# Kernel tuning notes

Hardware: AMD Instinct MI355X
Metric: run time of the kernel (lower is better)

Reference implementation:

```python
import jax, jax.numpy as jnp
import numpy as np
from jax import lax

B, T1, E, D, OUT = 4096, 127, 128, 128, 1


def setup_inputs() -> dict:
    key = jax.random.key(0)
    ks = jax.random.split(key, 16)
    s = lambda fan_in: 1.0 / np.sqrt(fan_in)
    inp = {
        "input_encoded": jax.random.normal(ks[0], (B, T1, E), jnp.float32),
        "y_history": jax.random.normal(ks[1], (B, T1), jnp.float32),
        # v_d: Linear(E -> 1)
        "v_d_w": jax.random.uniform(ks[2], (1, E), jnp.float32, -s(E), s(E)),
        "v_d_b": jax.random.uniform(ks[3], (1,), jnp.float32, -s(E), s(E)),
        # W_dhs: Linear(2D -> E)
        "W_dhs_w": jax.random.uniform(ks[4], (E, 2 * D), jnp.float32, -s(2 * D), s(2 * D)),
        "W_dhs_b": jax.random.uniform(ks[5], (E,), jnp.float32, -s(2 * D), s(2 * D)),
        # U_d: Linear(E -> E)
        "U_d_w": jax.random.uniform(ks[6], (E, E), jnp.float32, -s(E), s(E)),
        "U_d_b": jax.random.uniform(ks[7], (E,), jnp.float32, -s(E), s(E)),
        # w: Linear((1+E)*OUT -> OUT); torch code does w.weight.data.normal_()
        "w_w": jax.random.normal(ks[8], (OUT, (1 + E) * OUT), jnp.float32),
        "w_b": jax.random.uniform(ks[9], (OUT,), jnp.float32, -s((1 + E) * OUT), s((1 + E) * OUT)),
        # single-layer LSTM(input=OUT, hidden=D); gate order i,f,g,o
        "lstm_W_ih": jax.random.uniform(ks[10], (4 * D, OUT), jnp.float32, -s(D), s(D)),
        "lstm_W_hh": jax.random.uniform(ks[11], (4 * D, D), jnp.float32, -s(D), s(D)),
        "lstm_b_ih": jax.random.uniform(ks[12], (4 * D,), jnp.float32, -s(D), s(D)),
        "lstm_b_hh": jax.random.uniform(ks[13], (4 * D,), jnp.float32, -s(D), s(D)),
        # fc_final: Linear(D + OUT*E -> OUT)
        "fc_w": jax.random.uniform(ks[14], (OUT, D + OUT * E), jnp.float32, -s(D + OUT * E), s(D + OUT * E)),
        "fc_b": jax.random.uniform(ks[15], (OUT,), jnp.float32, -s(D + OUT * E), s(D + OUT * E)),
    }
    return inp


def reference(input_encoded, y_history, v_d_w, v_d_b, W_dhs_w, W_dhs_b,
              U_d_w, U_d_b, w_w, w_b, lstm_W_ih, lstm_W_hh, lstm_b_ih,
              lstm_b_hh, fc_w, fc_b):
    batch = input_encoded.shape[0]
    d = lstm_W_hh.shape[1]
    e = input_encoded.shape[2]
    # U_d applied to encoder outputs is step-independent: precompute once. [B,T1,E]
    U = input_encoded @ U_d_w.T + U_d_b

    def step(carry, y_t):
        h, c, _ = carry  # h,c: [B,D]
        # temporal attention over encoder timesteps
        proj = jnp.concatenate([h, c], axis=-1) @ W_dhs_w.T + W_dhs_b  # [B,E]
        scores = jnp.tanh(proj[:, None, :] + U) @ v_d_w[0] + v_d_b[0]  # [B,T1]
        beta = jax.nn.softmax(scores, axis=1)
        ctx = jnp.einsum('bt,bte->be', beta, input_encoded)  # [B,E]
        # y_tilde and one LSTM step
        y_tilde = jnp.concatenate([ctx, y_t[:, None]], axis=-1) @ w_w.T + w_b  # [B,1]
        gates = y_tilde @ lstm_W_ih.T + lstm_b_ih + h @ lstm_W_hh.T + lstm_b_hh
        i_g, f_g, g_g, o_g = jnp.split(gates, 4, axis=-1)
        c_new = jax.nn.sigmoid(f_g) * c + jax.nn.sigmoid(i_g) * jnp.tanh(g_g)
        h_new = jax.nn.sigmoid(o_g) * jnp.tanh(c_new)
        return (h_new, c_new, ctx), None

    h0 = jnp.zeros((batch, d), input_encoded.dtype)
    c0 = jnp.zeros((batch, d), input_encoded.dtype)
    ctx0 = jnp.zeros((batch, e), input_encoded.dtype)
    (h, c, ctx), _ = lax.scan(step, (h0, c0, ctx0), y_history.T)  # scan over T-1 steps
    y_pred = jnp.concatenate([h, ctx], axis=-1) @ fc_w.T + fc_b  # [B,1]
    return y_pred
```

## Files before the change

### kernel.cpp

```cpp
#include <hip/hip_runtime.h>
#include <hip/hip_bf16.h>

#if __has_builtin(__builtin_amdgcn_exp2f)
#define EXP2F(x) __builtin_amdgcn_exp2f(x)
#else
#define EXP2F(x) exp2f(x)
#endif
#if __has_builtin(__builtin_amdgcn_rcpf)
#define RCPF(x) __builtin_amdgcn_rcpf(x)
#else
#define RCPF(x) (1.0f/(x))
#endif

typedef _Float16 h2f16 __attribute__((ext_vector_type(2)));
typedef _Float16 f16x8 __attribute__((ext_vector_type(8)));
typedef float    f32x16 __attribute__((ext_vector_type(16)));

namespace {
constexpr int   kT   = 127;
constexpr int   kE   = 128;
constexpr int   kB   = 4096;
constexpr int   kNWG = 256;
constexpr int   kGRP = 4;
constexpr int   kBPW = 16;
constexpr float kLog2e = 1.4426950408889634f;
constexpr float kK2    = 2.8853900817779268f;
constexpr int   kSmemBytes = (32768 + 256 + 672) * 4 + (2064 + 6 * 512 + 128 + 256 + 132) * 4;

__device__ __forceinline__ unsigned int packf16(float a, float b) {
  h2f16 h = { (_Float16)a, (_Float16)b };
  return __builtin_bit_cast(unsigned int, h);
}

#if __has_builtin(__builtin_amdgcn_fdot2)
__device__ __forceinline__ float fdot2f(unsigned int a, unsigned int b, float c) {
  return __builtin_amdgcn_fdot2(__builtin_bit_cast(h2f16, a),
                                __builtin_bit_cast(h2f16, b), c, false);
}
#else
__device__ __forceinline__ float fdot2f(unsigned int a, unsigned int b, float c) {
  h2f16 ha = __builtin_bit_cast(h2f16, a), hb = __builtin_bit_cast(h2f16, b);
  return c + (float)ha.x * (float)hb.x + (float)ha.y * (float)hb.y;
}
#endif

template <int CTRL>
__device__ __forceinline__ float dppadd(float x) {
  return x + __int_as_float(__builtin_amdgcn_update_dpp(
      0, __float_as_int(x), CTRL, 0xF, 0xF, true));
}
template <int CTRL>
__device__ __forceinline__ float dppmov(float x) {
  return __int_as_float(__builtin_amdgcn_update_dpp(
      0, __float_as_int(x), CTRL, 0xF, 0xF, true));
}
__device__ __forceinline__ float redsum8dpp(float x) {
  x = dppadd<0xB1>(x); x = dppadd<0x4E>(x); x = dppadd<0x141>(x);
  return x;
}
__device__ __forceinline__ float redsum64dpp(float x) {
  x = dppadd<0xB1>(x); x = dppadd<0x4E>(x); x = dppadd<0x141>(x); x = dppadd<0x128>(x);
  x += __shfl_xor(x, 16, 64);
  x += __shfl_xor(x, 32, 64);
  return x;
}
__device__ __forceinline__ float redsum64(float a) {
#pragma unroll
  for (int m = 1; m < 64; m <<= 1) a += __shfl_xor(a, m, 64);
  return a;
}

__global__ __launch_bounds__(1024, 4) void decoder_kernel(
    const float* __restrict__ Xg,
    const float* __restrict__ yh,
    const float* __restrict__ vdw,
    const float* __restrict__ vdb,
    const float* __restrict__ Wdhs,
    const float* __restrict__ Wdhsb,
    const float* __restrict__ Udw,
    const float* __restrict__ Udb,
    const float* __restrict__ ww,
    const float* __restrict__ wb,
    const float* __restrict__ Wih,
    const float* __restrict__ Whh,
    const float* __restrict__ bih,
    const float* __restrict__ bhh,
    const float* __restrict__ fcww,
    const float* __restrict__ fcb,
    float* __restrict__ out)
{
  extern __shared__ char smem[];
  unsigned int* u2u  = (unsigned int*)smem;
  unsigned int* udw2 = u2u + 3 * 8192;
  unsigned int* p2h  = u2u + 4 * 8192;
  unsigned int* hc2  = p2h + 256;
  float* act  = (float*)(hc2 + 672);
  float* sc   = act  + 2064;
  float* XW   = sc   + 512;
  float* yc   = XW   + 512;
  float* beta = yc   + 512;
  float* hl   = beta + 512;
  float* ctxl = hl   + 512;
  float* udbl = ctxl + 512;
  float* fcw  = udbl + 128;
  float* wwl  = fcw  + 256;

  const int tid   = threadIdx.x;
  const int d8    = tid >> 3;
  const int sub   = tid & 7;
  const int gate  = sub >> 1;
  const int g     = gate * 128 + d8;
  const int lane  = tid & 63;

  unsigned int whhA[32];
  {
    const int wid = tid >> 6;
    const int rrA = lane & 31;
    const int rowA = (rrA & 3) * 128 + (8 * wid + (rrA >> 2));
    const int kbA = (lane >> 5) * 8;
#pragma unroll
    for (int kk = 0; kk < 8; ++kk)
#pragma unroll
      for (int i2 = 0; i2 < 4; ++i2) {
        const int k = kk * 16 + kbA + 2 * i2;
        whhA[kk * 4 + i2] = packf16(Whh[rowA * 128 + k], Whh[rowA * 128 + k + 1]);
      }
  }
  unsigned int wdq[16];
#pragma unroll
  for (int q = 0; q < 16; ++q)
    wdq[q] = packf16(Wdhs[d8 * 256 + sub * 32 + 2 * q],
                     Wdhs[d8 * 256 + sub * 32 + 2 * q + 1]);
  unsigned int v2p[8];
#pragma unroll
  for (int i = 0; i < 8; ++i)
    v2p[i] = packf16(-2.0f * vdw[sub * 16 + 2 * i], -2.0f * vdw[sub * 16 + 2 * i + 1]);
  float bihh = bih[g] + bhh[g];
  float wihr = Wih[g];
  float wdbp = Wdhsb[d8];
  const float a_c = (gate == 2) ? -2.0f : 1.0f;
  const float b_c = (gate == 2) ? kK2 : -kLog2e;
  const float c_c = (gate == 2) ? 1.0f : 0.0f;
#pragma unroll
  for (int p = 0; p < 32; ++p) asm volatile("" : "+v"(whhA[p]));
#pragma unroll
  for (int q = 0; q < 16; ++q) asm volatile("" : "+v"(wdq[q]));
#pragma unroll
  for (int i = 0; i < 8; ++i) asm volatile("" : "+v"(v2p[i]));
  asm volatile("" : "+v"(bihh));
  asm volatile("" : "+v"(wihr));
  asm volatile("" : "+v"(wdbp));

  if (tid < 132) wwl[tid] = (tid < 129) ? ww[tid] : ((tid == 129) ? wb[0] : 0.f);
  if (tid < 256) fcw[tid] = fcww[tid];
  if (tid < 128) udbl[tid] = Udb[tid];
  (void)vdb;

  for (int grp = 0; grp < kBPW / kGRP; ++grp) {
    const int b0 = blockIdx.x * kBPW + grp * kGRP;
    float creg[kGRP] = {0.f, 0.f, 0.f, 0.f};
    __syncthreads();

    {
      const int r = tid >> 3, mb = (tid & 7) * 2;
#pragma unroll
      for (int ch = 0; ch < 2; ++ch) {
        const int m = mb + ch;
        const float4 wa = *(const float4*)&Udw[r * kE + m * 8];
        const float4 wb4 = *(const float4*)&Udw[r * kE + m * 8 + 4];
        uint4 st;
        st.x = packf16(wa.x, wa.y);  st.y = packf16(wa.z, wa.w);
        st.z = packf16(wb4.x, wb4.y); st.w = packf16(wb4.z, wb4.w);
        *(uint4*)&udw2[r * 64 + ((m ^ (r >> 4)) << 2)] = st;
      }
    }
    if (tid < 672) hc2[tid] = 0u;
    if (tid < 512) {
      const int j = tid >> 7, s2 = tid & 127;
      yc[tid] = (s2 < kT) ? wwl[128] * yh[(size_t)(b0 + j) * kT + s2] + wwl[129] : 0.f;
      if (s2 == 127) XW[tid] = 0.f;
    }
    __syncthreads();

    uint4 st3a, st3b;
    if (d8 < kT) {
#pragma unroll
      for (int j = 0; j < kGRP; ++j) {
        const float* Xrow = Xg + (size_t)(b0 + j) * (kT * kE) + d8 * kE;
        float a = 0.f;
#pragma unroll
        for (int q = 0; q < 4; ++q) {
          const float4 xv = *(const float4*)&Xrow[sub * 16 + q * 4];
          const float4 wv = *(const float4*)&wwl[sub * 16 + q * 4];
          a += xv.x * wv.x + xv.y * wv.y + xv.z * wv.z + xv.w * wv.w;
        }
        a = redsum8dpp(a);
        if (sub == 0) XW[j * 128 + d8] = a;
        float acc[16];
#pragma unroll
        for (int jj = 0; jj < 16; ++jj) acc[jj] = 0.f;
        for (int m = 0; m < 16; ++m) {
          const float4 xa = *(const float4*)&Xrow[m * 8];
          const float4 xb4 = *(const float4*)&Xrow[m * 8 + 4];
          const unsigned int xp0 = packf16(xa.x, xa.y), xp1 = packf16(xa.z, xa.w);
          const unsigned int xp2 = packf16(xb4.x, xb4.y), xp3 = packf16(xb4.z, xb4.w);
#pragma unroll
          for (int jj = 0; jj < 16; ++jj) {
            const uint4 wq = *(const uint4*)&udw2[(sub * 16 + jj) * 64 + ((m ^ sub) << 2)];
            acc[jj] = fdot2f(xp3, wq.w, fdot2f(xp2, wq.z,
                      fdot2f(xp1, wq.y, fdot2f(xp0, wq.x, acc[jj]))));
          }
        }
        uint4 s0, s1;
        const int eb = sub * 16;
        s0.x = packf16(kK2 * (acc[0] + udbl[eb + 0]), kK2 * (acc[1] + udbl[eb + 1]));
        s0.y = packf16(kK2 * (acc[2] + udbl[eb + 2]), kK2 * (acc[3] + udbl[eb + 3]));
        s0.z = packf16(kK2 * (acc[4] + udbl[eb + 4]), kK2 * (acc[5] + udbl[eb + 5]));
        s0.w = packf16(kK2 * (acc[6] + udbl[eb + 6]), kK2 * (acc[7] + udbl[eb + 7]));
        s1.x = packf16(kK2 * (acc[8] + udbl[eb + 8]), kK2 * (acc[9] + udbl[eb + 9]));
        s1.y = packf16(kK2 * (acc[10] + udbl[eb + 10]), kK2 * (acc[11] + udbl[eb + 11]));
        s1.z = packf16(kK2 * (acc[12] + udbl[eb + 12]), kK2 * (acc[13] + udbl[eb + 13]));
        s1.w = packf16(kK2 * (acc[14] + udbl[eb + 14]), kK2 * (acc[15] + udbl[eb + 15]));
        if (j < 3) {
          *(uint4*)&u2u[j * 8192 + d8 * 64 + (((sub * 2 + 0) ^ (d8 & 15)) << 2)] = s0;
          *(uint4*)&u2u[j * 8192 + d8 * 64 + (((sub * 2 + 1) ^ (d8 & 15)) << 2)] = s1;
        } else { st3a = s0; st3b = s1; }
      }
    }
    __syncthreads();
    if (d8 < kT) {
      *(uint4*)&u2u[3 * 8192 + d8 * 64 + (((sub * 2 + 0) ^ (d8 & 15)) << 2)] = st3a;
      *(uint4*)&u2u[3 * 8192 + d8 * 64 + (((sub * 2 + 1) ^ (d8 & 15)) << 2)] = st3b;
    }

    for (int s = 0; s < kT; ++s) {
      {
        f32x16 macc;
#pragma unroll
        for (int i = 0; i < 16; ++i) macc[i] = 0.f;
        const int jn = tid & 3;
        const int hi4 = ((tid >> 5) & 1) * 4;
#pragma unroll
        for (int kk = 0; kk < 8; ++kk) {
          const int p0 = kk * 8 + hi4;
          const uint4 bq = *(const uint4*)&hc2[jn * 168 + (p0 >> 4) * 20 + (p0 & 15)];
          const uint4 aq = {whhA[kk * 4 + 0], whhA[kk * 4 + 1],
                            whhA[kk * 4 + 2], whhA[kk * 4 + 3]};
          macc = __builtin_amdgcn_mfma_f32_32x32x16_f16(
              __builtin_bit_cast(f16x8, aq), __builtin_bit_cast(f16x8, bq),
              macc, 0, 0, 0);
        }
        if ((tid & 31) < 4) {
          const int wid = tid >> 6;
#pragma unroll
          for (int qq = 0; qq < 4; ++qq) {
            float4 v = {macc[qq * 4 + 0], macc[qq * 4 + 1],
                        macc[qq * 4 + 2], macc[qq * 4 + 3]};
            *(float4*)&act[(tid & 3) * 516 + 32 * wid + 8 * qq + hi4] = v;
          }
        }
      }
#pragma unroll
      for (int j = 0; j < kGRP; ++j) {
        const unsigned int* hj = hc2 + j * 168;
        float pp = 0.f;
#pragma unroll
        for (int q = 0; q < 4; ++q) {
          const uint4 h4 = *(const uint4*)&hj[sub * 20 + q * 4];
          pp = fdot2f(wdq[q * 4 + 0], h4.x, pp);
          pp = fdot2f(wdq[q * 4 + 1], h4.y, pp);
          pp = fdot2f(wdq[q * 4 + 2], h4.z, pp);
          pp = fdot2f(wdq[q * 4 + 3], h4.w, pp);
        }
        pp = redsum8dpp(pp);
        const float pv = kK2 * (pp + wdbp);
        const float pvo = dppmov<0x128>(pv);
        if ((tid & 15) == 0) p2h[j * 64 + (d8 >> 1)] = packf16(pv, pvo);
      }
      __syncthreads();

      if (d8 < kT) {
        const int sw = d8 & 15;
#pragma unroll
        for (int j = 0; j < kGRP; ++j) {
          const unsigned int* ur = u2u + j * 8192 + d8 * 64;
          const unsigned int* ph = p2h + j * 64;
          const uint4 ua = *(const uint4*)&ur[(((sub * 2 + 0) ^ sw) << 2)];
          const uint4 ub = *(const uint4*)&ur[(((sub * 2 + 1) ^ sw) << 2)];
          const uint4 pa = *(const uint4*)&ph[sub * 8];
          const uint4 pb = *(const uint4*)&ph[sub * 8 + 4];
          const unsigned int uu[8] = {ua.x, ua.y, ua.z, ua.w, ub.x, ub.y, ub.z, ub.w};
          const unsigned int pp[8] = {pa.x, pa.y, pa.z, pa.w, pb.x, pb.y, pb.z, pb.w};
          float sacc = 0.f;
#pragma unroll
          for (int i = 0; i < 8; ++i) {
            const h2f16 xs = __builtin_bit_cast(h2f16, uu[i])
                           + __builtin_bit_cast(h2f16, pp[i]);
            const h2f16 vv = __builtin_bit_cast(h2f16, v2p[i]);
            sacc += (float)vv.x * RCPF(1.f + EXP2F((float)xs.x));
            sacc += (float)vv.y * RCPF(1.f + EXP2F((float)xs.y));
          }
          sacc = redsum8dpp(sacc);
          if (sub == 0) sc[j * 128 + d8] = sacc;
        }
      }
      __syncthreads();

      float rden4[kGRP];
      {
        float yt4[kGRP];
#pragma unroll
        for (int j = 0; j < kGRP; ++j) {
          const float e0v = EXP2F(sc[j * 128 + lane] * kLog2e);
          float e1v = 0.f, x1 = 0.f;
          if (lane < 63) {
            e1v = EXP2F(sc[j * 128 + 64 + lane] * kLog2e);
            x1 = XW[j * 128 + 64 + lane];
          }
          float num = e0v * XW[j * 128 + lane] + e1v * x1;
          float den = e0v + e1v;
          num = redsum64dpp(num);
          den = redsum64dpp(den);
          rden4[j] = RCPF(den);
          yt4[j] = num * rden4[j] + yc[j * 128 + s];
        }
#pragma unroll
        for (int j = 0; j < kGRP; ++j) {
          const float gdot = act[j * 516 + (d8 << 2) + gate];
          const float av = c_c + a_c * RCPF(1.f + EXP2F(b_c * (gdot + bihh + yt4[j] * wihr)));
          const float fv = __shfl_xor(av, 2, 64);
          const float gv = __shfl_xor(av, 4, 64);
          const float ov = __shfl_xor(av, 6, 64);
          const float cn = fv * creg[j] + av * gv;
          creg[j] = cn;
          const float th = 1.f - 2.f * RCPF(1.f + EXP2F(cn * kK2));
          const float hn = ov * th;
          const float ho = dppmov<0x128>(hn);
          const float co = dppmov<0x128>(cn);
          if ((tid & 15) == 0) {
            const int p = d8 >> 1;
            hc2[j * 168 + ((p >> 4)) * 20 + (p & 15)]       = packf16(hn, ho);
            hc2[j * 168 + (4 + (p >> 4)) * 20 + (p & 15)]   = packf16(cn, co);
          }
          if (s == kT - 1 && sub == 0) hl[j * 128 + d8] = hn;
        }
      }
      if (s == kT - 1 && tid < 512) {
        const int j = tid >> 7, t2 = tid & 127;
        const float rd = (j == 0) ? rden4[0] : (j == 1) ? rden4[1]
                       : (j == 2) ? rden4[2] : rden4[3];
        beta[tid] = (t2 < kT) ? EXP2F(sc[tid] * kLog2e) * rd : 0.f;
      }
      __syncthreads();
    }

    {
      const int j = tid >> 8, r = tid & 255, e = r >> 1, hf = r & 1;
      const float* Xbj = Xg + (size_t)(b0 + j) * (kT * kE);
      float cacc = 0.f;
#pragma unroll
      for (int i = 0; i < 64; ++i) {
        const int t2 = hf * 64 + i;
        if (t2 < kT) cacc += beta[j * 128 + t2] * Xbj[(size_t)t2 * kE + e];
      }
      cacc += __shfl_xor(cacc, 1, 64);
      if (hf == 0) ctxl[j * 128 + e] = cacc;
    }
    __syncthreads();
    if (tid < 256) {
      const int j = tid >> 6, l = tid & 63;
      float a2 = hl[j * 128 + l] * fcw[l] + hl[j * 128 + 64 + l] * fcw[64 + l]
               + ctxl[j * 128 + l] * fcw[128 + l] + ctxl[j * 128 + 64 + l] * fcw[192 + l];
      a2 = redsum64(a2);
      if (l == 0) out[b0 + j] = a2 + fcb[0];
    }
  }
}
}

extern "C" void kernel_launch(void* const* d_in, const int* in_sizes, int n_in,
                              void* d_out, int out_size, void* d_ws, size_t ws_size,
                              hipStream_t stream) {
  (void)in_sizes; (void)n_in; (void)d_ws; (void)ws_size; (void)out_size;
  const float* Xg    = (const float*)d_in[0];
  const float* yh    = (const float*)d_in[1];
  const float* vdw   = (const float*)d_in[2];
  const float* vdb   = (const float*)d_in[3];
  const float* Wdhs  = (const float*)d_in[4];
  const float* Wdhsb = (const float*)d_in[5];
  const float* Udw   = (const float*)d_in[6];
  const float* Udb   = (const float*)d_in[7];
  const float* ww    = (const float*)d_in[8];
  const float* wb    = (const float*)d_in[9];
  const float* Wih   = (const float*)d_in[10];
  const float* Whh   = (const float*)d_in[11];
  const float* bih   = (const float*)d_in[12];
  const float* bhh   = (const float*)d_in[13];
  const float* fcww  = (const float*)d_in[14];
  const float* fcb   = (const float*)d_in[15];
  float* out = (float*)d_out;

  hipFuncSetAttribute((const void*)decoder_kernel,
                      hipFuncAttributeMaxDynamicSharedMemorySize, kSmemBytes);
  decoder_kernel<<<dim3(kNWG), dim3(1024), kSmemBytes, stream>>>(
      Xg, yh, vdw, vdb, Wdhs, Wdhsb, Udw, Udb, ww, wb,
      Wih, Whh, bih, bhh, fcww, fcb, out);
}
```

Before: 4.724 ms.

## Compute attention hidden projection with MFMA and flatten LSTM gate update per thread

The per-step W_dhs projection of [h,c], previously done with fdot2 and DPP reductions in every thread, now runs as 32x32x16 f16 MFMAs on 8 waves. Weights are pre-scaled by the tanh constant and kept in registers, and the two K halves are written to separate buffers that the score stage adds together. The LSTM cell update is restructured so that one thread of 512 computes all four gates for a (batch, unit) pair from float4 loads. This removes the cross-lane gate shuffles and the redundant softmax reduction that every thread used to repeat. The cost is more LDS traffic, an extra f16 add per score element, some f16 precision loss from splitting the sum, and half the threads idle in the gate phase.

```diff
diff --git a/kernel.cpp b/kernel.cpp
--- a/kernel.cpp
+++ b/kernel.cpp
@@ -25,11 +25,15 @@
 constexpr int   kBPW = 16;
 constexpr float kLog2e = 1.4426950408889634f;
 constexpr float kK2    = 2.8853900817779268f;
-constexpr int   kSmemBytes = (32768 + 256 + 672) * 4 + (2064 + 6 * 512 + 128 + 256 + 132) * 4;
+constexpr int   kSmemBytes = (34080 + 6676) * 4;
 
 __device__ __forceinline__ unsigned int packf16(float a, float b) {
   h2f16 h = { (_Float16)a, (_Float16)b };
   return __builtin_bit_cast(unsigned int, h);
+}
+__device__ __forceinline__ unsigned int pkaddf16(unsigned int a, unsigned int b) {
+  h2f16 r = __builtin_bit_cast(h2f16, a) + __builtin_bit_cast(h2f16, b);
+  return __builtin_bit_cast(unsigned int, r);
 }
 
 #if __has_builtin(__builtin_amdgcn_fdot2)
@@ -90,11 +94,14 @@
     float* __restrict__ out)
 {
   extern __shared__ char smem[];
-  unsigned int* u2u  = (unsigned int*)smem;
-  unsigned int* udw2 = u2u + 3 * 8192;
-  unsigned int* p2h  = u2u + 4 * 8192;
-  unsigned int* hc2  = p2h + 256;
-  float* act  = (float*)(hc2 + 672);
+  unsigned int* u2u   = (unsigned int*)smem;
+  unsigned int* udw2  = u2u + 3 * 8192;
+  unsigned int* p2hA  = u2u + 4 * 8192;
+  unsigned int* p2hB  = p2hA + 256;
+  unsigned int* hc2   = p2hB + 256;
+  unsigned int* wdb2h = hc2 + 672;
+  unsigned int* v2h   = wdb2h + 64;
+  float* act  = (float*)(v2h + 64);
   float* sc   = act  + 2064;
   float* XW   = sc   + 512;
   float* yc   = XW   + 512;
@@ -104,13 +111,12 @@
   float* udbl = ctxl + 512;
   float* fcw  = udbl + 128;
   float* wwl  = fcw  + 256;
-
-  const int tid   = threadIdx.x;
-  const int d8    = tid >> 3;
-  const int sub   = tid & 7;
-  const int gate  = sub >> 1;
-  const int g     = gate * 128 + d8;
-  const int lane  = tid & 63;
+  float* biw  = wwl  + 132;
+
+  const int tid  = threadIdx.x;
+  const int d8   = tid >> 3;
+  const int sub  = tid & 7;
+  const int lane = tid & 63;
 
   unsigned int whhA[32];
   {
@@ -126,39 +132,43 @@
         whhA[kk * 4 + i2] = packf16(Whh[rowA * 128 + k], Whh[rowA * 128 + k + 1]);
       }
   }
-  unsigned int wdq[16];
-#pragma unroll
-  for (int q = 0; q < 16; ++q)
-    wdq[q] = packf16(Wdhs[d8 * 256 + sub * 32 + 2 * q],
-                     Wdhs[d8 * 256 + sub * 32 + 2 * q + 1]);
-  unsigned int v2p[8];
-#pragma unroll
-  for (int i = 0; i < 8; ++i)
-    v2p[i] = packf16(-2.0f * vdw[sub * 16 + 2 * i], -2.0f * vdw[sub * 16 + 2 * i + 1]);
-  float bihh = bih[g] + bhh[g];
-  float wihr = Wih[g];
-  float wdbp = Wdhsb[d8];
-  const float a_c = (gate == 2) ? -2.0f : 1.0f;
-  const float b_c = (gate == 2) ? kK2 : -kLog2e;
-  const float c_c = (gate == 2) ? 1.0f : 0.0f;
+  unsigned int whhP[32];
+  {
+    const int wid8 = (tid >> 6) & 7;
+    const int rt = wid8 & 3, kh = wid8 >> 2;
+    const int rowP = rt * 32 + (lane & 31);
+    const int kb = kh * 128 + (lane >> 5) * 8;
+#pragma unroll
+    for (int kk = 0; kk < 8; ++kk)
+#pragma unroll
+      for (int i2 = 0; i2 < 4; ++i2) {
+        const int k = kb + kk * 16 + 2 * i2;
+        whhP[kk * 4 + i2] = packf16(kK2 * Wdhs[rowP * 256 + k],
+                                    kK2 * Wdhs[rowP * 256 + k + 1]);
+      }
+  }
 #pragma unroll
   for (int p = 0; p < 32; ++p) asm volatile("" : "+v"(whhA[p]));
 #pragma unroll
-  for (int q = 0; q < 16; ++q) asm volatile("" : "+v"(wdq[q]));
-#pragma unroll
-  for (int i = 0; i < 8; ++i) asm volatile("" : "+v"(v2p[i]));
-  asm volatile("" : "+v"(bihh));
-  asm volatile("" : "+v"(wihr));
-  asm volatile("" : "+v"(wdbp));
+  for (int p = 0; p < 32; ++p) asm volatile("" : "+v"(whhP[p]));
 
   if (tid < 132) wwl[tid] = (tid < 129) ? ww[tid] : ((tid == 129) ? wb[0] : 0.f);
   if (tid < 256) fcw[tid] = fcww[tid];
   if (tid < 128) udbl[tid] = Udb[tid];
+  if (tid < 64) {
+    wdb2h[tid] = packf16(kK2 * Wdhsb[2 * tid], kK2 * Wdhsb[2 * tid + 1]);
+    v2h[tid]   = packf16(-2.0f * vdw[2 * tid], -2.0f * vdw[2 * tid + 1]);
+  }
+  if (tid < 512) {
+    const int dd = tid >> 2, gg = tid & 3;
+    biw[tid]       = bih[gg * 128 + dd] + bhh[gg * 128 + dd];
+    biw[512 + tid] = Wih[gg * 128 + dd];
+  }
   (void)vdb;
 
   for (int grp = 0; grp < kBPW / kGRP; ++grp) {
     const int b0 = blockIdx.x * kBPW + grp * kGRP;
-    float creg[kGRP] = {0.f, 0.f, 0.f, 0.f};
+    float creg = 0.f;
     __syncthreads();
 
     {
@@ -260,45 +270,70 @@
           }
         }
       }
-#pragma unroll
-      for (int j = 0; j < kGRP; ++j) {
-        const unsigned int* hj = hc2 + j * 168;
-        float pp = 0.f;
-#pragma unroll
-        for (int q = 0; q < 4; ++q) {
-          const uint4 h4 = *(const uint4*)&hj[sub * 20 + q * 4];
-          pp = fdot2f(wdq[q * 4 + 0], h4.x, pp);
-          pp = fdot2f(wdq[q * 4 + 1], h4.y, pp);
-          pp = fdot2f(wdq[q * 4 + 2], h4.z, pp);
-          pp = fdot2f(wdq[q * 4 + 3], h4.w, pp);
-        }
-        pp = redsum8dpp(pp);
-        const float pv = kK2 * (pp + wdbp);
-        const float pvo = dppmov<0x128>(pv);
-        if ((tid & 15) == 0) p2h[j * 64 + (d8 >> 1)] = packf16(pv, pvo);
+      if (tid < 512) {
+        f32x16 pacc;
+#pragma unroll
+        for (int i = 0; i < 16; ++i) pacc[i] = 0.f;
+        const int wid8 = tid >> 6;
+        const int rt = wid8 & 3, kh = wid8 >> 2;
+        const int jn = tid & 3;
+        const int hi = (tid >> 5) & 1;
+#pragma unroll
+        for (int kk = 0; kk < 8; ++kk) {
+          const int p0 = kh * 64 + kk * 8 + hi * 4;
+          const uint4 bq = *(const uint4*)&hc2[jn * 168 + (p0 >> 4) * 20 + (p0 & 15)];
+          const uint4 aq = {whhP[kk * 4 + 0], whhP[kk * 4 + 1],
+                            whhP[kk * 4 + 2], whhP[kk * 4 + 3]};
+          pacc = __builtin_amdgcn_mfma_f32_32x32x16_f16(
+              __builtin_bit_cast(f16x8, aq), __builtin_bit_cast(f16x8, bq),
+              pacc, 0, 0, 0);
+        }
+        if ((tid & 31) < 4) {
+          const int j = tid & 31;
+          unsigned int* dst = (kh == 0) ? p2hA : p2hB;
+#pragma unroll
+          for (int qq = 0; qq < 4; ++qq) {
+            const int pr0 = rt * 16 + 4 * qq + 2 * hi;
+            unsigned int pa0 = packf16(pacc[qq * 4 + 0], pacc[qq * 4 + 1]);
+            unsigned int pa1 = packf16(pacc[qq * 4 + 2], pacc[qq * 4 + 3]);
+            if (kh == 0) {
+              pa0 = pkaddf16(pa0, wdb2h[pr0]);
+              pa1 = pkaddf16(pa1, wdb2h[pr0 + 1]);
+            }
+            uint2 st = {pa0, pa1};
+            *(uint2*)&dst[j * 64 + pr0] = st;
+          }
+        }
       }
       __syncthreads();
 
       if (d8 < kT) {
         const int sw = d8 & 15;
+        const uint4 vqa = *(const uint4*)&v2h[sub * 8];
+        const uint4 vqb = *(const uint4*)&v2h[sub * 8 + 4];
+        const unsigned int vv[8] = {vqa.x, vqa.y, vqa.z, vqa.w,
+                                    vqb.x, vqb.y, vqb.z, vqb.w};
 #pragma unroll
         for (int j = 0; j < kGRP; ++j) {
           const unsigned int* ur = u2u + j * 8192 + d8 * 64;
-          const unsigned int* ph = p2h + j * 64;
           const uint4 ua = *(const uint4*)&ur[(((sub * 2 + 0) ^ sw) << 2)];
           const uint4 ub = *(const uint4*)&ur[(((sub * 2 + 1) ^ sw) << 2)];
-          const uint4 pa = *(const uint4*)&ph[sub * 8];
-          const uint4 pb = *(const uint4*)&ph[sub * 8 + 4];
+          const uint4 pa = *(const uint4*)&p2hA[j * 64 + sub * 8];
+          const uint4 pb = *(const uint4*)&p2hA[j * 64 + sub * 8 + 4];
+          const uint4 qa = *(const uint4*)&p2hB[j * 64 + sub * 8];
+          const uint4 qb = *(const uint4*)&p2hB[j * 64 + sub * 8 + 4];
           const unsigned int uu[8] = {ua.x, ua.y, ua.z, ua.w, ub.x, ub.y, ub.z, ub.w};
           const unsigned int pp[8] = {pa.x, pa.y, pa.z, pa.w, pb.x, pb.y, pb.z, pb.w};
+          const unsigned int qq2[8] = {qa.x, qa.y, qa.z, qa.w, qb.x, qb.y, qb.z, qb.w};
           float sacc = 0.f;
 #pragma unroll
           for (int i = 0; i < 8; ++i) {
             const h2f16 xs = __builtin_bit_cast(h2f16, uu[i])
-                           + __builtin_bit_cast(h2f16, pp[i]);
-            const h2f16 vv = __builtin_bit_cast(h2f16, v2p[i]);
-            sacc += (float)vv.x * RCPF(1.f + EXP2F((float)xs.x));
-            sacc += (float)vv.y * RCPF(1.f + EXP2F((float)xs.y));
+                           + __builtin_bit_cast(h2f16, pp[i])
+                           + __builtin_bit_cast(h2f16, qq2[i]);
+            const h2f16 vx = __builtin_bit_cast(h2f16, vv[i]);
+            sacc += (float)vx.x * RCPF(1.f + EXP2F((float)xs.x));
+            sacc += (float)vx.y * RCPF(1.f + EXP2F((float)xs.y));
           }
           sacc = redsum8dpp(sacc);
           if (sub == 0) sc[j * 128 + d8] = sacc;
@@ -306,50 +341,42 @@
       }
       __syncthreads();
 
-      float rden4[kGRP];
-      {
-        float yt4[kGRP];
-#pragma unroll
-        for (int j = 0; j < kGRP; ++j) {
-          const float e0v = EXP2F(sc[j * 128 + lane] * kLog2e);
-          float e1v = 0.f, x1 = 0.f;
-          if (lane < 63) {
-            e1v = EXP2F(sc[j * 128 + 64 + lane] * kLog2e);
-            x1 = XW[j * 128 + 64 + lane];
-          }
-          float num = e0v * XW[j * 128 + lane] + e1v * x1;
-          float den = e0v + e1v;
-          num = redsum64dpp(num);
-          den = redsum64dpp(den);
-          rden4[j] = RCPF(den);
-          yt4[j] = num * rden4[j] + yc[j * 128 + s];
-        }
-#pragma unroll
-        for (int j = 0; j < kGRP; ++j) {
-          const float gdot = act[j * 516 + (d8 << 2) + gate];
-          const float av = c_c + a_c * RCPF(1.f + EXP2F(b_c * (gdot + bihh + yt4[j] * wihr)));
-          const float fv = __shfl_xor(av, 2, 64);
-          const float gv = __shfl_xor(av, 4, 64);
-          const float ov = __shfl_xor(av, 6, 64);
-          const float cn = fv * creg[j] + av * gv;
-          creg[j] = cn;
-          const float th = 1.f - 2.f * RCPF(1.f + EXP2F(cn * kK2));
-          const float hn = ov * th;
-          const float ho = dppmov<0x128>(hn);
-          const float co = dppmov<0x128>(cn);
-          if ((tid & 15) == 0) {
-            const int p = d8 >> 1;
-            hc2[j * 168 + ((p >> 4)) * 20 + (p & 15)]       = packf16(hn, ho);
-            hc2[j * 168 + (4 + (p >> 4)) * 20 + (p & 15)]   = packf16(cn, co);
-          }
-          if (s == kT - 1 && sub == 0) hl[j * 128 + d8] = hn;
-        }
-      }
-      if (s == kT - 1 && tid < 512) {
-        const int j = tid >> 7, t2 = tid & 127;
-        const float rd = (j == 0) ? rden4[0] : (j == 1) ? rden4[1]
-                       : (j == 2) ? rden4[2] : rden4[3];
-        beta[tid] = (t2 < kT) ? EXP2F(sc[tid] * kLog2e) * rd : 0.f;
+      if (tid < 512) {
+        const int j = tid >> 7, dd = tid & 127, ln = tid & 63;
+        const float e0v = EXP2F(sc[j * 128 + ln] * kLog2e);
+        float e1v = 0.f, x1 = 0.f;
+        if (ln < 63) {
+          e1v = EXP2F(sc[j * 128 + 64 + ln] * kLog2e);
+          x1 = XW[j * 128 + 64 + ln];
+        }
+        float num = e0v * XW[j * 128 + ln] + e1v * x1;
+        float den = e0v + e1v;
+        num = redsum64dpp(num);
+        den = redsum64dpp(den);
+        const float rden = RCPF(den);
+        const float yt = num * rden + yc[j * 128 + s];
+        const float4 a4 = *(const float4*)&act[j * 516 + 4 * dd];
+        const float4 bi = *(const float4*)&biw[4 * dd];
+        const float4 wi = *(const float4*)&biw[512 + 4 * dd];
+        const float si = RCPF(1.f + EXP2F(-(a4.x + bi.x + yt * wi.x) * kLog2e));
+        const float sf = RCPF(1.f + EXP2F(-(a4.y + bi.y + yt * wi.y) * kLog2e));
+        const float tg = 1.f - 2.f * RCPF(1.f + EXP2F((a4.z + bi.z + yt * wi.z) * kK2));
+        const float so = RCPF(1.f + EXP2F(-(a4.w + bi.w + yt * wi.w) * kLog2e));
+        const float cn = sf * creg + si * tg;
+        creg = cn;
+        const float th = 1.f - 2.f * RCPF(1.f + EXP2F(cn * kK2));
+        const float hn = so * th;
+        const float ho = dppmov<0xB1>(hn);
+        const float co = dppmov<0xB1>(cn);
+        if ((tid & 1) == 0) {
+          const int p = dd >> 1;
+          hc2[j * 168 + (p >> 4) * 20 + (p & 15)]       = packf16(hn, ho);
+          hc2[j * 168 + (4 + (p >> 4)) * 20 + (p & 15)] = packf16(cn, co);
+        }
+        if (s == kT - 1) {
+          hl[j * 128 + dd] = hn;
+          beta[tid] = (dd < kT) ? EXP2F(sc[tid] * kLog2e) * rden : 0.f;
+        }
       }
       __syncthreads();
     }
```

After: 4.000 ms. -15.3%, faster.
